# Optimization experiments

Measured on AMD Instinct MI355X. Metric: run time of the kernel, lower is better.

## Reference

```python
import jax, jax.numpy as jnp
import numpy as np

N_NODES = 100000
N_EDGES = 1600000
DIN = 128
DOUT = 128
N_SUP = 2


def setup_inputs() -> dict:
    key = jax.random.key(0)
    k = jax.random.split(key, 6)
    x = jax.random.normal(k[0], (N_NODES, DIN), dtype=jnp.float32)
    w = jax.random.normal(k[1], (N_SUP, DIN, DOUT), dtype=jnp.float32) * (1.0 / np.sqrt(DIN))
    bias = jax.random.normal(k[2], (DOUT,), dtype=jnp.float32) * 0.01
    sup_vals = jax.random.uniform(k[3], (N_SUP, N_EDGES), dtype=jnp.float32)
    sup_rows = jax.random.randint(k[4], (N_SUP, N_EDGES), 0, N_NODES, dtype=jnp.int32)
    sup_cols = jax.random.randint(k[5], (N_SUP, N_EDGES), 0, N_NODES, dtype=jnp.int32)
    return {"x": x, "w": w, "bias": bias, "sup_vals": sup_vals,
            "sup_rows": sup_rows, "sup_cols": sup_cols}


def _spmm(vals, rows, cols, dense):
    # COO sparse [N,N] @ dense [N,D] -> [N,D]
    gathered = vals[:, None] * dense[cols]        # [E, D]
    return jax.ops.segment_sum(gathered, rows, num_segments=N_NODES)


def reference(x, w, bias, sup_vals, sup_rows, sup_cols):
    # pre_sup_i = x @ w_i for each support: [S, N, Dout]
    pre = jnp.einsum('nd,sdo->sno', x, w)
    # SpMM per support, vmapped over the support axis, then summed
    supports = jax.vmap(_spmm)(sup_vals, sup_rows, sup_cols, pre)  # [S, N, Dout]
    out = supports.sum(axis=0) + bias
    return jax.nn.relu(out)
```

## Files before the change

### kernel.cpp

```cpp
#include <hip/hip_runtime.h>

#define N_NODES 100000
#define N_EDGES 1600000
#define DIN 128
#define DOUT 128
#define N_SUP 2
#define E_TOT (N_SUP * N_EDGES)

#define BIN_ROWS 128
#define BSHIFT 7
#define NBINS ((N_NODES + BIN_ROWS - 1) / BIN_ROWS)

#define SC_EPT 16
#define SC_BLOCK 256
#define SC_CHUNK (SC_EPT * SC_BLOCK)
#define NBLK_SC ((E_TOT + SC_CHUNK - 1) / SC_CHUNK)

#define GEMM_ROWS 128
#define LDK 136

typedef float        f32x2 __attribute__((ext_vector_type(2)));
typedef float        f32x4 __attribute__((ext_vector_type(4)));
typedef unsigned int u32;
typedef u32          u32x2 __attribute__((ext_vector_type(2)));
typedef u32          u32x4 __attribute__((ext_vector_type(4)));
typedef short        bf16x8 __attribute__((ext_vector_type(8)));

static __device__ __forceinline__ u32 pack_bf16x2(float lo, float hi) {
    u32 ul = __float_as_uint(lo);
    u32 uh = __float_as_uint(hi);
    ul = (ul + 0x7FFFu + ((ul >> 16) & 1u)) >> 16;
    uh = ((uh + 0x7FFFu + ((uh >> 16) & 1u)) >> 16) << 16;
    return ul | uh;
}

__global__ __launch_bounds__(256) void wconv_kernel(const float* __restrict__ w,
                                                    u32* __restrict__ wTb) {
    const int s = blockIdx.x;
    const int n = threadIdx.x >> 1;
    const int kh = (threadIdx.x & 1) * 64;
    const float* wp = w + (size_t)s * DIN * DOUT + n;
    u32 o[32];
    #pragma unroll
    for (int j = 0; j < 32; j++) {
        const float lo = wp[(size_t)(kh + 2 * j) * DOUT];
        const float hi = wp[(size_t)(kh + 2 * j + 1) * DOUT];
        o[j] = pack_bf16x2(lo, hi);
    }
    u32* op = wTb + ((size_t)s * 128 + n) * 64 + kh / 2;
    #pragma unroll
    for (int j = 0; j < 8; j++)
        *(u32x4*)(op + j * 4) = *(u32x4*)&o[j * 4];
}

__global__ __launch_bounds__(256) void mfma_gemm_kernel(const float* __restrict__ x,
                                                        const u32* __restrict__ wTb,
                                                        u32* __restrict__ pre) {
    __shared__ alignas(16) unsigned short stage[2][GEMM_ROWS][LDK];
    float (*epi)[129] = (float (*)[129])(void*)stage;

    const int s = blockIdx.y;
    const int row0 = blockIdx.x * GEMM_ROWS;
    const int t = threadIdx.x;
    const int lane = t & 63;
    const int wv = t >> 6;

    {
        const int r = t >> 1;
        const int half = t & 1;
        const int gr = row0 + r;
        u32* dst = (u32*)&stage[0][r][half * 64];
        u32 o[32];
        if (gr < N_NODES) {
            const float* p = x + (size_t)gr * DIN + half * 64;
            #pragma unroll
            for (int j = 0; j < 16; j++) {
                const f32x4 a = *(const f32x4*)(p + j * 4);
                o[2 * j]     = pack_bf16x2(a.x, a.y);
                o[2 * j + 1] = pack_bf16x2(a.z, a.w);
            }
        } else {
            #pragma unroll
            for (int j = 0; j < 32; j++) o[j] = 0;
        }
        #pragma unroll
        for (int j = 0; j < 8; j++)
            *(u32x4*)(dst + j * 4) = *(u32x4*)&o[j * 4];
        const u32* wp = wTb + ((size_t)s * 128 + r) * 64 + half * 32;
        u32* wdst = (u32*)&stage[1][r][half * 64];
        #pragma unroll
        for (int j = 0; j < 8; j++)
            *(u32x4*)(wdst + j * 4) = *(const u32x4*)(wp + j * 4);
    }
    __syncthreads();

    const int q = lane >> 4;
    const int ml = lane & 15;
    const int m0 = wv * 32;

    f32x4 acc[2][8];
    #pragma unroll
    for (int mt = 0; mt < 2; mt++)
        #pragma unroll
        for (int nt = 0; nt < 8; nt++) acc[mt][nt] = (f32x4){0.f, 0.f, 0.f, 0.f};

    #pragma unroll
    for (int kt = 0; kt < 4; kt++) {
        const int k0 = kt * 32 + q * 8;
        const bf16x8 a0 = *(const bf16x8*)&stage[0][m0 + ml][k0];
        const bf16x8 a1 = *(const bf16x8*)&stage[0][m0 + 16 + ml][k0];
        #pragma unroll
        for (int nt = 0; nt < 8; nt++) {
            const bf16x8 b = *(const bf16x8*)&stage[1][nt * 16 + ml][k0];
            acc[0][nt] = __builtin_amdgcn_mfma_f32_16x16x32_bf16(a0, b, acc[0][nt], 0, 0, 0);
            acc[1][nt] = __builtin_amdgcn_mfma_f32_16x16x32_bf16(a1, b, acc[1][nt], 0, 0, 0);
        }
    }
    __syncthreads();

    #pragma unroll
    for (int mt = 0; mt < 2; mt++)
        #pragma unroll
        for (int nt = 0; nt < 8; nt++)
            #pragma unroll
            for (int r = 0; r < 4; r++)
                epi[m0 + mt * 16 + q * 4 + r][nt * 16 + ml] = acc[mt][nt][r];
    __syncthreads();

    {
        const int row = t >> 1;
        const int half = t & 1;
        const int gr = row0 + row;
        if (gr < N_NODES) {
            u32 ov[32];
            #pragma unroll
            for (int j = 0; j < 32; j++)
                ov[j] = pack_bf16x2(epi[row][half * 64 + 2 * j],
                                    epi[row][half * 64 + 2 * j + 1]);
            u32* op = pre + ((size_t)s * N_NODES + gr) * 64 + half * 32;
            #pragma unroll
            for (int j = 0; j < 8; j++)
                __builtin_nontemporal_store(*(u32x4*)&ov[j * 4], (u32x4*)(op + j * 4));
        }
    }
}

__global__ __launch_bounds__(256) void binhist_kernel(const int* __restrict__ rows,
                                                      int* __restrict__ bin_cnt) {
    __shared__ int h[NBINS];
    const int t = threadIdx.x;
    for (int i = t; i < NBINS; i += 256) h[i] = 0;
    __syncthreads();
    const int base = blockIdx.x * SC_CHUNK;
    #pragma unroll
    for (int j = 0; j < SC_EPT; j++) {
        const int i = base + j * 256 + t;
        if (i < E_TOT) atomicAdd(&h[__builtin_nontemporal_load(rows + i) >> BSHIFT], 1);
    }
    __syncthreads();
    for (int i = t; i < NBINS; i += 256)
        if (h[i]) atomicAdd(&bin_cnt[i], h[i]);
}

__global__ __launch_bounds__(1024) void binscan_kernel(const int* __restrict__ bin_cnt,
                                                       int* __restrict__ bin_base,
                                                       int* __restrict__ bin_cursor) {
    __shared__ int s[1024];
    const int t = threadIdx.x;
    const int v = (t < NBINS) ? bin_cnt[t] : 0;
    s[t] = v;
    __syncthreads();
    #pragma unroll
    for (int off = 1; off < 1024; off <<= 1) {
        const int u = (t >= off) ? s[t - off] : 0;
        __syncthreads();
        s[t] += u;
        __syncthreads();
    }
    if (t < NBINS) {
        const int ex = s[t] - v;
        bin_base[t] = ex;
        bin_cursor[t] = ex;
    }
    if (t == 0) bin_base[NBINS] = E_TOT;
}

__global__ __launch_bounds__(256) void binscatter_kernel(const int* __restrict__ rows,
                                                         const int* __restrict__ cols,
                                                         const float* __restrict__ vals,
                                                         int* __restrict__ bin_cursor,
                                                         u32x2* __restrict__ edata) {
    __shared__ int lcnt[NBINS];
    __shared__ int lbase[NBINS];
    const int t = threadIdx.x;
    for (int i = t; i < NBINS; i += 256) lcnt[i] = 0;
    __syncthreads();

    const int base = blockIdx.x * SC_CHUNK;
    int bin[SC_EPT], lpos[SC_EPT];
    u32x2 pay[SC_EPT];
    #pragma unroll
    for (int j = 0; j < SC_EPT; j++) {
        const int i = base + j * 256 + t;
        if (i < E_TOT) {
            const int r = __builtin_nontemporal_load(rows + i);
            const int c = __builtin_nontemporal_load(cols + i);
            const float v = __builtin_nontemporal_load(vals + i);
            const int b = r >> BSHIFT;
            bin[j] = b;
            lpos[j] = atomicAdd(&lcnt[b], 1);
            pay[j].x = (u32)(c + ((i >= N_EDGES) ? N_NODES : 0)) |
                       ((u32)(r & (BIN_ROWS - 1)) << 18);
            pay[j].y = __float_as_uint(v);
        } else {
            bin[j] = -1;
        }
    }
    __syncthreads();
    for (int b = t; b < NBINS; b += 256) {
        const int c = lcnt[b];
        if (c) lbase[b] = atomicAdd(&bin_cursor[b], c);
    }
    __syncthreads();
    #pragma unroll
    for (int j = 0; j < SC_EPT; j++) {
        if (bin[j] >= 0) edata[lbase[bin[j]] + lpos[j]] = pay[j];
    }
}

__global__ __launch_bounds__(256) void binsort_kernel(const u32x2* __restrict__ edata,
                                                      u32x2* __restrict__ edata2,
                                                      const int* __restrict__ bin_base,
                                                      int* __restrict__ row_start) {
    __shared__ int rcnt[BIN_ROWS];
    __shared__ int rscan[BIN_ROWS];
    const int t = threadIdx.x;
    const int b = blockIdx.x;
    const int beg = bin_base[b];
    const int end = bin_base[b + 1];

    if (t < BIN_ROWS) rcnt[t] = 0;
    __syncthreads();
    for (int e = beg + t; e < end; e += 256)
        atomicAdd(&rcnt[edata[e].x >> 18], 1);
    __syncthreads();

    const int v = (t < BIN_ROWS) ? rcnt[t] : 0;
    if (t < BIN_ROWS) rscan[t] = v;
    __syncthreads();
    #pragma unroll
    for (int off = 1; off < BIN_ROWS; off <<= 1) {
        const int u = (t < BIN_ROWS && t >= off) ? rscan[t - off] : 0;
        __syncthreads();
        if (t < BIN_ROWS) rscan[t] += u;
        __syncthreads();
    }
    if (t < BIN_ROWS) {
        const int ex = rscan[t] - v;
        rcnt[t] = ex;
        const int row = b * BIN_ROWS + t;
        if (row < N_NODES) row_start[row] = beg + ex;
    }
    __syncthreads();
    for (int e = beg + t; e < end; e += 256) {
        const u32x2 d = edata[e];
        const int pos = beg + atomicAdd(&rcnt[d.x >> 18], 1);
        u32x2 o;
        o.x = d.x & 0x3FFFFu;
        o.y = d.y;
        edata2[pos] = o;
    }
    if (b == NBINS - 1 && t == 0) row_start[N_NODES] = E_TOT;
}

__global__ __launch_bounds__(256, 6) void gather_kernel(const u32* __restrict__ pre,
                                                        const u32x2* __restrict__ edata2,
                                                        const int* __restrict__ row_start,
                                                        const float* __restrict__ bias,
                                                        float* __restrict__ out) {
    const int lane = threadIdx.x & 63;
    const int wid = threadIdx.x >> 6;
    const int row = blockIdx.x * 4 + wid;
    if (row >= N_NODES) return;

    const int beg = row_start[row];
    const int end = row_start[row + 1];

    float ax = 0.f, ay = 0.f;
    int e = beg;

    if (e + 8 <= end) {
        u32x2 d[8];
        #pragma unroll
        for (int j = 0; j < 8; j++)
            d[j] = __builtin_nontemporal_load(edata2 + e + j);
        for (;;) {
            u32 u[8];
            #pragma unroll
            for (int j = 0; j < 8; j++)
                u[j] = pre[(u32)((d[j].x << 6) + (u32)lane)];
            const int en = e + 8;
            const bool more = (en + 8 <= end);
            u32x2 dn[8];
            if (more) {
                #pragma unroll
                for (int j = 0; j < 8; j++)
                    dn[j] = __builtin_nontemporal_load(edata2 + en + j);
            }
            #pragma unroll
            for (int j = 0; j < 8; j++) {
                const float v = __uint_as_float(d[j].y);
                ax = fmaf(v, __uint_as_float(u[j] << 16), ax);
                ay = fmaf(v, __uint_as_float(u[j] & 0xFFFF0000u), ay);
            }
            e = en;
            if (!more) break;
            #pragma unroll
            for (int j = 0; j < 8; j++) d[j] = dn[j];
        }
    }
    for (; e + 4 <= end; e += 4) {
        u32x2 d[4];
        #pragma unroll
        for (int j = 0; j < 4; j++)
            d[j] = __builtin_nontemporal_load(edata2 + e + j);
        u32 u[4];
        #pragma unroll
        for (int j = 0; j < 4; j++)
            u[j] = pre[(u32)((d[j].x << 6) + (u32)lane)];
        #pragma unroll
        for (int j = 0; j < 4; j++) {
            const float v = __uint_as_float(d[j].y);
            ax = fmaf(v, __uint_as_float(u[j] << 16), ax);
            ay = fmaf(v, __uint_as_float(u[j] & 0xFFFF0000u), ay);
        }
    }
    for (; e < end; e++) {
        const u32x2 d = __builtin_nontemporal_load(edata2 + e);
        const u32 u = pre[(u32)((d.x << 6) + (u32)lane)];
        const float v = __uint_as_float(d.y);
        ax = fmaf(v, __uint_as_float(u << 16), ax);
        ay = fmaf(v, __uint_as_float(u & 0xFFFF0000u), ay);
    }

    const float2 b = *(const float2*)(bias + lane * 2);
    f32x2 r;
    r.x = fmaxf(ax + b.x, 0.f);
    r.y = fmaxf(ay + b.y, 0.f);
    __builtin_nontemporal_store(r, (f32x2*)(out + (size_t)row * DOUT + lane * 2));
}

extern "C" void kernel_launch(void* const* d_in, const int* in_sizes, int n_in,
                              void* d_out, int out_size, void* d_ws, size_t ws_size,
                              hipStream_t stream) {
    (void)in_sizes; (void)n_in; (void)out_size; (void)ws_size;
    const float* x        = (const float*)d_in[0];
    const float* w        = (const float*)d_in[1];
    const float* bias     = (const float*)d_in[2];
    const float* sup_vals = (const float*)d_in[3];
    const int*   sup_rows = (const int*)d_in[4];
    const int*   sup_cols = (const int*)d_in[5];
    float* out = (float*)d_out;

    char* ws = (char*)d_ws;
    u32*   pre       = (u32*)ws;
    u32x2* edata     = (u32x2*)(ws + (size_t)N_SUP * N_NODES * 64 * 4);
    u32x2* edata2    = (u32x2*)((char*)edata + (size_t)E_TOT * 8);
    int*   bin_cnt   = (int*)((char*)edata2 + (size_t)E_TOT * 8);
    int*   bin_base  = bin_cnt + NBINS;
    int*   bin_cursor= bin_base + NBINS + 1;
    int*   row_start = bin_cursor + NBINS;
    u32*   wTb       = (u32*)(row_start + N_NODES + 1);

    wconv_kernel<<<N_SUP, 256, 0, stream>>>(w, wTb);
    {
        dim3 grid((N_NODES + GEMM_ROWS - 1) / GEMM_ROWS, N_SUP);
        mfma_gemm_kernel<<<grid, 256, 0, stream>>>(x, wTb, pre);
    }
    (void)hipMemsetAsync(bin_cnt, 0, NBINS * sizeof(int), stream);
    binhist_kernel<<<NBLK_SC, 256, 0, stream>>>(sup_rows, bin_cnt);
    binscan_kernel<<<1, 1024, 0, stream>>>(bin_cnt, bin_base, bin_cursor);
    binscatter_kernel<<<NBLK_SC, 256, 0, stream>>>(sup_rows, sup_cols, sup_vals,
                                                   bin_cursor, edata);
    binsort_kernel<<<NBINS, 256, 0, stream>>>(edata, edata2, bin_base, row_start);
    gather_kernel<<<(N_NODES + 3) / 4, 256, 0, stream>>>(pre, edata2, row_start, bias, out);
}
```

Measured before the change: 432.3 us.

## Replace two-level bin sort with direct per-row atomic CSR build

Drops the bin histogram, bin scatter and per-bin row sort in favour of a global per-row histogram, a single-block scan over all rows, and a scatter that places edges via per-row atomic cursors. This removes one full pass over the edge array and an intermediate buffer. In exchange it uses many global atomics and fully random scatter writes, and the order of edges within a row becomes nondeterministic.

New measurement: 915.2 us. 112% more time.

```diff
diff --git a/kernel.cpp b/kernel.cpp
--- a/kernel.cpp
+++ b/kernel.cpp
@@ -7,10 +7,6 @@
 #define N_SUP 2
 #define E_TOT (N_SUP * N_EDGES)
 
-#define BIN_ROWS 128
-#define BSHIFT 7
-#define NBINS ((N_NODES + BIN_ROWS - 1) / BIN_ROWS)
-
 #define SC_EPT 16
 #define SC_BLOCK 256
 #define SC_CHUNK (SC_EPT * SC_BLOCK)
@@ -18,6 +14,8 @@
 
 #define GEMM_ROWS 128
 #define LDK 136
+
+#define SCAN_CHUNK 98
 
 typedef float        f32x2 __attribute__((ext_vector_type(2)));
 typedef float        f32x4 __attribute__((ext_vector_type(4)));
@@ -145,30 +143,29 @@
     }
 }
 
-__global__ __launch_bounds__(256) void binhist_kernel(const int* __restrict__ rows,
-                                                      int* __restrict__ bin_cnt) {
-    __shared__ int h[NBINS];
+__global__ __launch_bounds__(256) void ghist_kernel(const int* __restrict__ rows,
+                                                    int* __restrict__ row_cnt) {
+    const int base = blockIdx.x * SC_CHUNK;
     const int t = threadIdx.x;
-    for (int i = t; i < NBINS; i += 256) h[i] = 0;
-    __syncthreads();
-    const int base = blockIdx.x * SC_CHUNK;
     #pragma unroll
     for (int j = 0; j < SC_EPT; j++) {
         const int i = base + j * 256 + t;
-        if (i < E_TOT) atomicAdd(&h[__builtin_nontemporal_load(rows + i) >> BSHIFT], 1);
-    }
-    __syncthreads();
-    for (int i = t; i < NBINS; i += 256)
-        if (h[i]) atomicAdd(&bin_cnt[i], h[i]);
-}
-
-__global__ __launch_bounds__(1024) void binscan_kernel(const int* __restrict__ bin_cnt,
-                                                       int* __restrict__ bin_base,
-                                                       int* __restrict__ bin_cursor) {
+        if (i < E_TOT)
+            atomicAdd(&row_cnt[__builtin_nontemporal_load(rows + i)], 1);
+    }
+}
+
+__global__ __launch_bounds__(1024) void gscan_kernel(const int* __restrict__ row_cnt,
+                                                     int* __restrict__ row_start,
+                                                     int* __restrict__ row_cursor) {
     __shared__ int s[1024];
     const int t = threadIdx.x;
-    const int v = (t < NBINS) ? bin_cnt[t] : 0;
-    s[t] = v;
+    const int r0 = t * SCAN_CHUNK;
+    const int r1 = min(r0 + SCAN_CHUNK, N_NODES);
+
+    int sum = 0;
+    for (int r = r0; r < r1; r++) sum += row_cnt[r];
+    s[t] = sum;
     __syncthreads();
     #pragma unroll
     for (int off = 1; off < 1024; off <<= 1) {
@@ -177,28 +174,22 @@
         s[t] += u;
         __syncthreads();
     }
-    if (t < NBINS) {
-        const int ex = s[t] - v;
-        bin_base[t] = ex;
-        bin_cursor[t] = ex;
-    }
-    if (t == 0) bin_base[NBINS] = E_TOT;
-}
-
-__global__ __launch_bounds__(256) void binscatter_kernel(const int* __restrict__ rows,
-                                                         const int* __restrict__ cols,
-                                                         const float* __restrict__ vals,
-                                                         int* __restrict__ bin_cursor,
-                                                         u32x2* __restrict__ edata) {
-    __shared__ int lcnt[NBINS];
-    __shared__ int lbase[NBINS];
+    int run = s[t] - sum;
+    for (int r = r0; r < r1; r++) {
+        row_start[r] = run;
+        row_cursor[r] = run;
+        run += row_cnt[r];
+    }
+    if (t == 1023) row_start[N_NODES] = E_TOT;
+}
+
+__global__ __launch_bounds__(256) void gscatter_kernel(const int* __restrict__ rows,
+                                                       const int* __restrict__ cols,
+                                                       const float* __restrict__ vals,
+                                                       int* __restrict__ row_cursor,
+                                                       u32x2* __restrict__ edata2) {
+    const int base = blockIdx.x * SC_CHUNK;
     const int t = threadIdx.x;
-    for (int i = t; i < NBINS; i += 256) lcnt[i] = 0;
-    __syncthreads();
-
-    const int base = blockIdx.x * SC_CHUNK;
-    int bin[SC_EPT], lpos[SC_EPT];
-    u32x2 pay[SC_EPT];
     #pragma unroll
     for (int j = 0; j < SC_EPT; j++) {
         const int i = base + j * 256 + t;
@@ -206,71 +197,13 @@
             const int r = __builtin_nontemporal_load(rows + i);
             const int c = __builtin_nontemporal_load(cols + i);
             const float v = __builtin_nontemporal_load(vals + i);
-            const int b = r >> BSHIFT;
-            bin[j] = b;
-            lpos[j] = atomicAdd(&lcnt[b], 1);
-            pay[j].x = (u32)(c + ((i >= N_EDGES) ? N_NODES : 0)) |
-                       ((u32)(r & (BIN_ROWS - 1)) << 18);
-            pay[j].y = __float_as_uint(v);
-        } else {
-            bin[j] = -1;
-        }
-    }
-    __syncthreads();
-    for (int b = t; b < NBINS; b += 256) {
-        const int c = lcnt[b];
-        if (c) lbase[b] = atomicAdd(&bin_cursor[b], c);
-    }
-    __syncthreads();
-    #pragma unroll
-    for (int j = 0; j < SC_EPT; j++) {
-        if (bin[j] >= 0) edata[lbase[bin[j]] + lpos[j]] = pay[j];
-    }
-}
-
-__global__ __launch_bounds__(256) void binsort_kernel(const u32x2* __restrict__ edata,
-                                                      u32x2* __restrict__ edata2,
-                                                      const int* __restrict__ bin_base,
-                                                      int* __restrict__ row_start) {
-    __shared__ int rcnt[BIN_ROWS];
-    __shared__ int rscan[BIN_ROWS];
-    const int t = threadIdx.x;
-    const int b = blockIdx.x;
-    const int beg = bin_base[b];
-    const int end = bin_base[b + 1];
-
-    if (t < BIN_ROWS) rcnt[t] = 0;
-    __syncthreads();
-    for (int e = beg + t; e < end; e += 256)
-        atomicAdd(&rcnt[edata[e].x >> 18], 1);
-    __syncthreads();
-
-    const int v = (t < BIN_ROWS) ? rcnt[t] : 0;
-    if (t < BIN_ROWS) rscan[t] = v;
-    __syncthreads();
-    #pragma unroll
-    for (int off = 1; off < BIN_ROWS; off <<= 1) {
-        const int u = (t < BIN_ROWS && t >= off) ? rscan[t - off] : 0;
-        __syncthreads();
-        if (t < BIN_ROWS) rscan[t] += u;
-        __syncthreads();
-    }
-    if (t < BIN_ROWS) {
-        const int ex = rscan[t] - v;
-        rcnt[t] = ex;
-        const int row = b * BIN_ROWS + t;
-        if (row < N_NODES) row_start[row] = beg + ex;
-    }
-    __syncthreads();
-    for (int e = beg + t; e < end; e += 256) {
-        const u32x2 d = edata[e];
-        const int pos = beg + atomicAdd(&rcnt[d.x >> 18], 1);
-        u32x2 o;
-        o.x = d.x & 0x3FFFFu;
-        o.y = d.y;
-        edata2[pos] = o;
-    }
-    if (b == NBINS - 1 && t == 0) row_start[N_NODES] = E_TOT;
+            const int pos = atomicAdd(&row_cursor[r], 1);
+            u32x2 o;
+            o.x = (u32)(c + ((i >= N_EDGES) ? N_NODES : 0));
+            o.y = __float_as_uint(v);
+            edata2[pos] = o;
+        }
+    }
 }
 
 __global__ __launch_bounds__(256, 6) void gather_kernel(const u32* __restrict__ pre,
@@ -364,24 +297,21 @@
 
     char* ws = (char*)d_ws;
     u32*   pre       = (u32*)ws;
-    u32x2* edata     = (u32x2*)(ws + (size_t)N_SUP * N_NODES * 64 * 4);
-    u32x2* edata2    = (u32x2*)((char*)edata + (size_t)E_TOT * 8);
-    int*   bin_cnt   = (int*)((char*)edata2 + (size_t)E_TOT * 8);
-    int*   bin_base  = bin_cnt + NBINS;
-    int*   bin_cursor= bin_base + NBINS + 1;
-    int*   row_start = bin_cursor + NBINS;
-    u32*   wTb       = (u32*)(row_start + N_NODES + 1);
+    u32x2* edata2    = (u32x2*)(ws + (size_t)N_SUP * N_NODES * 64 * 4);
+    int*   row_cnt   = (int*)((char*)edata2 + (size_t)E_TOT * 8);
+    int*   row_start = row_cnt + N_NODES + 1;
+    int*   row_cursor= row_start + N_NODES + 1;
+    u32*   wTb       = (u32*)(row_cursor + N_NODES);
 
     wconv_kernel<<<N_SUP, 256, 0, stream>>>(w, wTb);
     {
         dim3 grid((N_NODES + GEMM_ROWS - 1) / GEMM_ROWS, N_SUP);
         mfma_gemm_kernel<<<grid, 256, 0, stream>>>(x, wTb, pre);
     }
-    (void)hipMemsetAsync(bin_cnt, 0, NBINS * sizeof(int), stream);
-    binhist_kernel<<<NBLK_SC, 256, 0, stream>>>(sup_rows, bin_cnt);
-    binscan_kernel<<<1, 1024, 0, stream>>>(bin_cnt, bin_base, bin_cursor);
-    binscatter_kernel<<<NBLK_SC, 256, 0, stream>>>(sup_rows, sup_cols, sup_vals,
-                                                   bin_cursor, edata);
-    binsort_kernel<<<NBINS, 256, 0, stream>>>(edata, edata2, bin_base, row_start);
+    (void)hipMemsetAsync(row_cnt, 0, (N_NODES + 1) * sizeof(int), stream);
+    ghist_kernel<<<NBLK_SC, 256, 0, stream>>>(sup_rows, row_cnt);
+    gscan_kernel<<<1, 1024, 0, stream>>>(row_cnt, row_start, row_cursor);
+    gscatter_kernel<<<NBLK_SC, 256, 0, stream>>>(sup_rows, sup_cols, sup_vals,
+                                                 row_cursor, edata2);
     gather_kernel<<<(N_NODES + 3) / 4, 256, 0, stream>>>(pre, edata2, row_start, bias, out);
 }
```

## Use fixed-capacity bins to drop histogram and scan passes, sort in LDS

Applied to the files above, without the earlier changes.

Replaces the exact per-bin histogram, memset and scan with fixed-capacity bin slots initialized by a tiny kernel, so edges are scattered directly without a prior counting pass over rows. The bin sort now stages each bin in shared memory and writes the sorted result in place, removing the second edge buffer, and emits per-row begin/end pairs. This saves a full read of the row indices and two launches, but relies on no bin exceeding the capacity; overflow would corrupt neighboring bins since the scatter does not bound-check.

Result: faster. 391.7 us (-9.4%).

```diff
diff --git a/kernel.cpp b/kernel.cpp
--- a/kernel.cpp
+++ b/kernel.cpp
@@ -10,6 +10,7 @@
 #define BIN_ROWS 128
 #define BSHIFT 7
 #define NBINS ((N_NODES + BIN_ROWS - 1) / BIN_ROWS)
+#define CAP 4608
 
 #define SC_EPT 16
 #define SC_BLOCK 256
@@ -145,44 +146,9 @@
     }
 }
 
-__global__ __launch_bounds__(256) void binhist_kernel(const int* __restrict__ rows,
-                                                      int* __restrict__ bin_cnt) {
-    __shared__ int h[NBINS];
-    const int t = threadIdx.x;
-    for (int i = t; i < NBINS; i += 256) h[i] = 0;
-    __syncthreads();
-    const int base = blockIdx.x * SC_CHUNK;
-    #pragma unroll
-    for (int j = 0; j < SC_EPT; j++) {
-        const int i = base + j * 256 + t;
-        if (i < E_TOT) atomicAdd(&h[__builtin_nontemporal_load(rows + i) >> BSHIFT], 1);
-    }
-    __syncthreads();
-    for (int i = t; i < NBINS; i += 256)
-        if (h[i]) atomicAdd(&bin_cnt[i], h[i]);
-}
-
-__global__ __launch_bounds__(1024) void binscan_kernel(const int* __restrict__ bin_cnt,
-                                                       int* __restrict__ bin_base,
-                                                       int* __restrict__ bin_cursor) {
-    __shared__ int s[1024];
-    const int t = threadIdx.x;
-    const int v = (t < NBINS) ? bin_cnt[t] : 0;
-    s[t] = v;
-    __syncthreads();
-    #pragma unroll
-    for (int off = 1; off < 1024; off <<= 1) {
-        const int u = (t >= off) ? s[t - off] : 0;
-        __syncthreads();
-        s[t] += u;
-        __syncthreads();
-    }
-    if (t < NBINS) {
-        const int ex = s[t] - v;
-        bin_base[t] = ex;
-        bin_cursor[t] = ex;
-    }
-    if (t == 0) bin_base[NBINS] = E_TOT;
+__global__ __launch_bounds__(256) void initcur_kernel(int* __restrict__ bin_cursor) {
+    const int b = blockIdx.x * 256 + threadIdx.x;
+    if (b < NBINS) bin_cursor[b] = b * CAP;
 }
 
 __global__ __launch_bounds__(256) void binscatter_kernel(const int* __restrict__ rows,
@@ -228,21 +194,24 @@
     }
 }
 
-__global__ __launch_bounds__(256) void binsort_kernel(const u32x2* __restrict__ edata,
-                                                      u32x2* __restrict__ edata2,
-                                                      const int* __restrict__ bin_base,
-                                                      int* __restrict__ row_start) {
+__global__ __launch_bounds__(256) void binsort_kernel(u32x2* __restrict__ edata,
+                                                      const int* __restrict__ bin_cursor,
+                                                      int2* __restrict__ rbe) {
+    __shared__ u32x2 ebuf[CAP];
     __shared__ int rcnt[BIN_ROWS];
     __shared__ int rscan[BIN_ROWS];
     const int t = threadIdx.x;
     const int b = blockIdx.x;
-    const int beg = bin_base[b];
-    const int end = bin_base[b + 1];
-
+    const int beg = b * CAP;
+    const int cnt = min(bin_cursor[b] - beg, CAP);
+
+    for (int e = t; e < cnt; e += 256)
+        ebuf[e] = __builtin_nontemporal_load(edata + beg + e);
     if (t < BIN_ROWS) rcnt[t] = 0;
     __syncthreads();
-    for (int e = beg + t; e < end; e += 256)
-        atomicAdd(&rcnt[edata[e].x >> 18], 1);
+
+    for (int e = t; e < cnt; e += 256)
+        atomicAdd(&rcnt[ebuf[e].x >> 18], 1);
     __syncthreads();
 
     const int v = (t < BIN_ROWS) ? rcnt[t] : 0;
@@ -259,23 +228,27 @@
         const int ex = rscan[t] - v;
         rcnt[t] = ex;
         const int row = b * BIN_ROWS + t;
-        if (row < N_NODES) row_start[row] = beg + ex;
-    }
-    __syncthreads();
-    for (int e = beg + t; e < end; e += 256) {
-        const u32x2 d = edata[e];
+        if (row < N_NODES) {
+            int2 be;
+            be.x = beg + ex;
+            be.y = beg + ex + v;
+            rbe[row] = be;
+        }
+    }
+    __syncthreads();
+    for (int e = t; e < cnt; e += 256) {
+        const u32x2 d = ebuf[e];
         const int pos = beg + atomicAdd(&rcnt[d.x >> 18], 1);
         u32x2 o;
         o.x = d.x & 0x3FFFFu;
         o.y = d.y;
-        edata2[pos] = o;
-    }
-    if (b == NBINS - 1 && t == 0) row_start[N_NODES] = E_TOT;
+        edata[pos] = o;
+    }
 }
 
 __global__ __launch_bounds__(256, 6) void gather_kernel(const u32* __restrict__ pre,
-                                                        const u32x2* __restrict__ edata2,
-                                                        const int* __restrict__ row_start,
+                                                        const u32x2* __restrict__ edata,
+                                                        const int2* __restrict__ rbe,
                                                         const float* __restrict__ bias,
                                                         float* __restrict__ out) {
     const int lane = threadIdx.x & 63;
@@ -283,17 +256,17 @@
     const int row = blockIdx.x * 4 + wid;
     if (row >= N_NODES) return;
 
-    const int beg = row_start[row];
-    const int end = row_start[row + 1];
+    const int2 be = rbe[row];
+    int e = be.x;
+    const int end = be.y;
 
     float ax = 0.f, ay = 0.f;
-    int e = beg;
 
     if (e + 8 <= end) {
         u32x2 d[8];
         #pragma unroll
         for (int j = 0; j < 8; j++)
-            d[j] = __builtin_nontemporal_load(edata2 + e + j);
+            d[j] = __builtin_nontemporal_load(edata + e + j);
         for (;;) {
             u32 u[8];
             #pragma unroll
@@ -305,7 +278,7 @@
             if (more) {
                 #pragma unroll
                 for (int j = 0; j < 8; j++)
-                    dn[j] = __builtin_nontemporal_load(edata2 + en + j);
+                    dn[j] = __builtin_nontemporal_load(edata + en + j);
             }
             #pragma unroll
             for (int j = 0; j < 8; j++) {
@@ -323,7 +296,7 @@
         u32x2 d[4];
         #pragma unroll
         for (int j = 0; j < 4; j++)
-            d[j] = __builtin_nontemporal_load(edata2 + e + j);
+            d[j] = __builtin_nontemporal_load(edata + e + j);
         u32 u[4];
         #pragma unroll
         for (int j = 0; j < 4; j++)
@@ -336,7 +309,7 @@
         }
     }
     for (; e < end; e++) {
-        const u32x2 d = __builtin_nontemporal_load(edata2 + e);
+        const u32x2 d = __builtin_nontemporal_load(edata + e);
         const u32 u = pre[(u32)((d.x << 6) + (u32)lane)];
         const float v = __uint_as_float(d.y);
         ax = fmaf(v, __uint_as_float(u << 16), ax);
@@ -365,23 +338,18 @@
     char* ws = (char*)d_ws;
     u32*   pre       = (u32*)ws;
     u32x2* edata     = (u32x2*)(ws + (size_t)N_SUP * N_NODES * 64 * 4);
-    u32x2* edata2    = (u32x2*)((char*)edata + (size_t)E_TOT * 8);
-    int*   bin_cnt   = (int*)((char*)edata2 + (size_t)E_TOT * 8);
-    int*   bin_base  = bin_cnt + NBINS;
-    int*   bin_cursor= bin_base + NBINS + 1;
-    int*   row_start = bin_cursor + NBINS;
-    u32*   wTb       = (u32*)(row_start + N_NODES + 1);
+    int2*  rbe       = (int2*)((char*)edata + (size_t)NBINS * CAP * 8);
+    int*   bin_cursor= (int*)(rbe + N_NODES);
+    u32*   wTb       = (u32*)(bin_cursor + NBINS + 2);
 
     wconv_kernel<<<N_SUP, 256, 0, stream>>>(w, wTb);
     {
         dim3 grid((N_NODES + GEMM_ROWS - 1) / GEMM_ROWS, N_SUP);
         mfma_gemm_kernel<<<grid, 256, 0, stream>>>(x, wTb, pre);
     }
-    (void)hipMemsetAsync(bin_cnt, 0, NBINS * sizeof(int), stream);
-    binhist_kernel<<<NBLK_SC, 256, 0, stream>>>(sup_rows, bin_cnt);
-    binscan_kernel<<<1, 1024, 0, stream>>>(bin_cnt, bin_base, bin_cursor);
+    initcur_kernel<<<(NBINS + 255) / 256, 256, 0, stream>>>(bin_cursor);
     binscatter_kernel<<<NBLK_SC, 256, 0, stream>>>(sup_rows, sup_cols, sup_vals,
                                                    bin_cursor, edata);
-    binsort_kernel<<<NBINS, 256, 0, stream>>>(edata, edata2, bin_base, row_start);
-    gather_kernel<<<(N_NODES + 3) / 4, 256, 0, stream>>>(pre, edata2, row_start, bias, out);
-}
+    binsort_kernel<<<NBINS, 256, 0, stream>>>(edata, bin_cursor, rbe);
+    gather_kernel<<<(N_NODES + 3) / 4, 256, 0, stream>>>(pre, edata, rbe, bias, out);
+}
```
